# Kernel optimization log

Measured on AMD Instinct MI355X. Metric: run time of the kernel, lower is better.

The kernel has to match this reference:

```python
import jax, jax.numpy as jnp
import numpy as np

N, E = 20000, 160000
D_IN, HID, HEADS = 256, 64, 10
NEG_SLOPE = 0.2


def setup_inputs() -> dict:
    key = jax.random.key(0)
    ks = jax.random.split(key, 12)
    s = 0.05
    f = jnp.float32
    return {
        "x": jax.random.normal(ks[0], (N, D_IN), f),
        "edge_index": jax.random.randint(ks[1], (2, E), 0, N, jnp.int32),
        # GATConv 1: in=D_IN, out=HID, heads=10, concat=True
        "W1": (jax.random.normal(ks[2], (D_IN, HEADS * HID), f) * s),
        "a_src1": (jax.random.normal(ks[3], (HEADS, HID), f) * s),
        "a_dst1": (jax.random.normal(ks[4], (HEADS, HID), f) * s),
        "b1": jnp.zeros((HEADS * HID,), f),
        # GATConv 2: in=HEADS*HID, out=HID, heads=1
        "W2": (jax.random.normal(ks[5], (HEADS * HID, HID), f) * s),
        "a_src2": (jax.random.normal(ks[6], (1, HID), f) * s),
        "a_dst2": (jax.random.normal(ks[7], (1, HID), f) * s),
        "b2": jnp.zeros((HID,), f),
        # final Linear(hidden_dim, hidden_dim)
        "Wfc": (jax.random.normal(ks[8], (HID, HID), f) * s),
        "bfc": jnp.zeros((HID,), f),
    }


def gat_conv(x, src, dst, n, W, a_src, a_dst, b, heads, concat):
    """PyG GATConv (eval mode): gather, leaky-relu scores, segment softmax, scatter."""
    c = W.shape[1] // heads
    h = (x @ W).reshape(n, heads, c)                      # [N, H, C]
    score_src = jnp.sum(h * a_src, axis=-1)               # [N, H]
    score_dst = jnp.sum(h * a_dst, axis=-1)               # [N, H]
    e = jax.nn.leaky_relu(score_src[src] + score_dst[dst], NEG_SLOPE)  # [E, H]
    # segment softmax over incoming edges of each dst node
    m = jax.ops.segment_max(e, dst, num_segments=n)
    e = jnp.exp(e - m[dst])
    denom = jax.ops.segment_sum(e, dst, num_segments=n)
    alpha = e / (denom[dst] + 1e-16)                      # [E, H]
    msg = alpha[:, :, None] * h[src]                      # [E, H, C]
    out = jax.ops.segment_sum(msg, dst, num_segments=n)   # [N, H, C]
    out = out.reshape(n, heads * c) if concat else out.mean(axis=1)
    return out + b


def reference(x, edge_index, W1, a_src1, a_dst1, b1, W2, a_src2, a_dst2, b2, Wfc, bfc):
    n = x.shape[0]
    # add self loops (PyG default)
    loops = jnp.arange(n, dtype=edge_index.dtype)
    src = jnp.concatenate([edge_index[0], loops])
    dst = jnp.concatenate([edge_index[1], loops])
    h = jax.nn.relu(gat_conv(x, src, dst, n, W1, a_src1, a_dst1, b1, HEADS, True))
    h = jax.nn.relu(gat_conv(h, src, dst, n, W2, a_src2, a_dst2, b2, 1, True))
    return jax.nn.relu(h @ Wfc + bfc)
```

## Files before the change

kernel.cpp:

```cpp
#include <hip/hip_runtime.h>
#include <cstdint>
#include <cstddef>

constexpr int N_NODES = 20000;
constexpr int E_EDGES = 160000;
constexpr int D_INC   = 256;
constexpr int HEADSC  = 10;
constexpr int EN      = E_EDGES + N_NODES;
constexpr int ELLW    = 96;
constexpr float NEG_SLOPE = 0.2f;

typedef _Float16 half8 __attribute__((ext_vector_type(8)));
typedef _Float16 half4v __attribute__((ext_vector_type(4)));
typedef float f32x4 __attribute__((ext_vector_type(4)));

typedef const __attribute__((address_space(1))) void* gas_ptr;
typedef __attribute__((address_space(3))) void* las_ptr;

__global__ __launch_bounds__(256) void gemm1_k(
    const _Float16* __restrict__ A,
    const _Float16* __restrict__ BT,
    _Float16* __restrict__ C,
    const float* __restrict__ asv, const float* __restrict__ adv,
    float* __restrict__ s_s, float* __restrict__ s_d, int M)
{
    __shared__ alignas(16) _Float16 Ah[128][64];
    __shared__ alignas(16) _Float16 Bh[128][64];
    const int tid = threadIdx.x;
    const int wv  = tid >> 6;
    const int ln  = tid & 63;
    const int wr  = wv >> 1;
    const int wc  = wv & 1;
    const int row0 = blockIdx.y * 128;
    const int col0 = blockIdx.x * 128;
    const int m = ln & 15;
    const int q = ln >> 4;
    const int srow = tid >> 3;
    const int sk   = (tid & 7) * 8;

    f32x4 acc[4][4] = {};

    for (int k0 = 0; k0 < 256; k0 += 64) {
#pragma unroll
        for (int u = 0; u < 4; ++u) {
            const int ar = min(row0 + u * 32 + srow, M - 1);
            __builtin_amdgcn_global_load_lds(
                (gas_ptr)(A + (size_t)ar * 256 + k0 + sk),
                (las_ptr)(&Ah[u * 32 + srow][sk]), 16, 0, 0);
        }
#pragma unroll
        for (int u = 0; u < 4; ++u) {
            __builtin_amdgcn_global_load_lds(
                (gas_ptr)(BT + (size_t)(col0 + u * 32 + srow) * 256 + k0 + sk),
                (las_ptr)(&Bh[u * 32 + srow][sk]), 16, 0, 0);
        }
        __syncthreads();

#pragma unroll
        for (int ks = 0; ks < 2; ++ks) {
            half8 af[4], bf[4];
#pragma unroll
            for (int i = 0; i < 4; ++i)
                af[i] = *reinterpret_cast<const half8*>(
                    &Ah[wr * 64 + i * 16 + m][ks * 32 + q * 8]);
#pragma unroll
            for (int j = 0; j < 4; ++j)
                bf[j] = *reinterpret_cast<const half8*>(
                    &Bh[wc * 64 + j * 16 + m][ks * 32 + q * 8]);
#pragma unroll
            for (int i = 0; i < 4; ++i)
#pragma unroll
                for (int j = 0; j < 4; ++j)
                    acc[i][j] = __builtin_amdgcn_mfma_f32_16x16x32_f16(
                        af[i], bf[j], acc[i][j], 0, 0, 0);
        }
        __syncthreads();
    }

#pragma unroll
    for (int i = 0; i < 4; ++i) {
#pragma unroll
        for (int j = 0; j < 4; ++j) {
            const int col = col0 + wc * 64 + j * 16 + m;
#pragma unroll
            for (int r = 0; r < 4; ++r) {
                const int row = row0 + wr * 64 + i * 16 + q * 4 + r;
                if (row < M)
                    C[(size_t)row * 640 + col] = (_Float16)acc[i][j][r];
            }
        }
    }

    const int hh = blockIdx.x * 2 + wc;
    float pa[4][4] = {}, pd[4][4] = {};
#pragma unroll
    for (int j = 0; j < 4; ++j) {
        const float a_ = asv[hh * 64 + j * 16 + m];
        const float d_ = adv[hh * 64 + j * 16 + m];
#pragma unroll
        for (int i = 0; i < 4; ++i)
#pragma unroll
            for (int r = 0; r < 4; ++r) {
                pa[i][r] += acc[i][j][r] * a_;
                pd[i][r] += acc[i][j][r] * d_;
            }
    }
#pragma unroll
    for (int o = 1; o < 16; o <<= 1) {
#pragma unroll
        for (int i = 0; i < 4; ++i)
#pragma unroll
            for (int r = 0; r < 4; ++r) {
                pa[i][r] += __shfl_xor(pa[i][r], o, 64);
                pd[i][r] += __shfl_xor(pd[i][r], o, 64);
            }
    }
    if (m == 0) {
#pragma unroll
        for (int i = 0; i < 4; ++i)
#pragma unroll
            for (int r = 0; r < 4; ++r) {
                const int row = row0 + wr * 64 + i * 16 + q * 4 + r;
                if (row < M) {
                    s_s[row * HEADSC + hh] = pa[i][r];
                    s_d[row * HEADSC + hh] = pd[i][r];
                }
            }
    }
}

__global__ __launch_bounds__(128) void gemm2_k(
    const _Float16* __restrict__ A,
    const _Float16* __restrict__ BT,
    _Float16* __restrict__ C,
    const float* __restrict__ asv, const float* __restrict__ adv,
    float* __restrict__ s_s, float* __restrict__ s_d)
{
    __shared__ alignas(16) _Float16 Ah[32][72];
    __shared__ alignas(16) _Float16 Bh[64][72];
    const int tid = threadIdx.x;
    const int wv  = tid >> 6;
    const int ln  = tid & 63;
    const int row0 = blockIdx.x * 32;
    const int m = ln & 15;
    const int q = ln >> 4;
    const int arow = tid >> 2;
    const int acg  = (tid & 3) * 16;
    const int brow = tid >> 1;
    const int bcg  = (tid & 1) * 32;

    const _Float16* aptr = A  + (size_t)(row0 + arow) * 640 + acg;
    const _Float16* bptr = BT + (size_t)brow * 640 + bcg;

    int4 a0, a1, b0, b1, b2, b3;
    a0 = *reinterpret_cast<const int4*>(aptr);
    a1 = *reinterpret_cast<const int4*>(aptr + 8);
    b0 = *reinterpret_cast<const int4*>(bptr);
    b1 = *reinterpret_cast<const int4*>(bptr + 8);
    b2 = *reinterpret_cast<const int4*>(bptr + 16);
    b3 = *reinterpret_cast<const int4*>(bptr + 24);

    f32x4 acc[4] = {};

    for (int k0 = 0; k0 < 640; k0 += 64) {
        *reinterpret_cast<int4*>(&Ah[arow][acg])      = a0;
        *reinterpret_cast<int4*>(&Ah[arow][acg + 8])  = a1;
        *reinterpret_cast<int4*>(&Bh[brow][bcg])      = b0;
        *reinterpret_cast<int4*>(&Bh[brow][bcg + 8])  = b1;
        *reinterpret_cast<int4*>(&Bh[brow][bcg + 16]) = b2;
        *reinterpret_cast<int4*>(&Bh[brow][bcg + 24]) = b3;
        __syncthreads();

        if (k0 + 64 < 640) {
            const _Float16* ap = aptr + k0 + 64;
            a0 = *reinterpret_cast<const int4*>(ap);
            a1 = *reinterpret_cast<const int4*>(ap + 8);
            const _Float16* bp = bptr + k0 + 64;
            b0 = *reinterpret_cast<const int4*>(bp);
            b1 = *reinterpret_cast<const int4*>(bp + 8);
            b2 = *reinterpret_cast<const int4*>(bp + 16);
            b3 = *reinterpret_cast<const int4*>(bp + 24);
        }

#pragma unroll
        for (int ks = 0; ks < 2; ++ks) {
            const half8 af = *reinterpret_cast<const half8*>(
                &Ah[wv * 16 + m][ks * 32 + q * 8]);
#pragma unroll
            for (int ct = 0; ct < 4; ++ct) {
                const half8 bf = *reinterpret_cast<const half8*>(
                    &Bh[ct * 16 + m][ks * 32 + q * 8]);
                acc[ct] = __builtin_amdgcn_mfma_f32_16x16x32_f16(af, bf, acc[ct],
                                                                 0, 0, 0);
            }
        }
        __syncthreads();
    }

#pragma unroll
    for (int ct = 0; ct < 4; ++ct) {
#pragma unroll
        for (int r = 0; r < 4; ++r) {
            const int row = row0 + wv * 16 + q * 4 + r;
            C[(size_t)row * 64 + ct * 16 + m] = (_Float16)acc[ct][r];
        }
    }

    float pa[4] = {}, pd[4] = {};
#pragma unroll
    for (int ct = 0; ct < 4; ++ct) {
        const float a_ = asv[ct * 16 + m];
        const float d_ = adv[ct * 16 + m];
#pragma unroll
        for (int r = 0; r < 4; ++r) {
            pa[r] += acc[ct][r] * a_;
            pd[r] += acc[ct][r] * d_;
        }
    }
#pragma unroll
    for (int o = 1; o < 16; o <<= 1) {
#pragma unroll
        for (int r = 0; r < 4; ++r) {
            pa[r] += __shfl_xor(pa[r], o, 64);
            pd[r] += __shfl_xor(pd[r], o, 64);
        }
    }
    if (m == 0) {
#pragma unroll
        for (int r = 0; r < 4; ++r) {
            const int row = row0 + wv * 16 + q * 4 + r;
            s_s[row] = pa[r];
            s_d[row] = pd[r];
        }
    }
}

constexpr int XQ   = N_NODES * D_INC / 4;
constexpr int W1E  = D_INC * 640;
constexpr int W2E  = 640 * 64;
constexpr int WFCE = 64 * 64;
constexpr int SETUP_TOT = EN + XQ + W1E + W2E + WFCE;

__global__ void setup_k(const int* __restrict__ src, const int* __restrict__ dst,
                        int* __restrict__ deg, int* __restrict__ ell,
                        const float* __restrict__ x, const float* __restrict__ W1,
                        const float* __restrict__ W2, const float* __restrict__ Wfc,
                        _Float16* __restrict__ x16, _Float16* __restrict__ W1T,
                        _Float16* __restrict__ W2T, _Float16* __restrict__ WfcT)
{
    const int i = blockIdx.x * 256 + threadIdx.x;
    if (i < EN) {
        const int base = deg[N_NODES];
        int d, s;
        if (i < E_EDGES) { d = dst[i]; s = src[i]; }
        else             { d = i - E_EDGES; s = d; }
        const int r = atomicAdd(&deg[d], 1) - base;
        if ((unsigned)r < (unsigned)ELLW) ell[(size_t)d * ELLW + r] = s;
    } else if (i < EN + XQ) {
        const int j = i - EN;
        const float4 v = reinterpret_cast<const float4*>(x)[j];
        half4v o = {(_Float16)v.x, (_Float16)v.y, (_Float16)v.z, (_Float16)v.w};
        reinterpret_cast<half4v*>(x16)[j] = o;
    } else if (i < EN + XQ + W1E) {
        const int j = i - EN - XQ;
        const int k = j / 640, n = j - k * 640;
        W1T[(size_t)n * D_INC + k] = (_Float16)W1[j];
    } else if (i < EN + XQ + W1E + W2E) {
        const int j = i - EN - XQ - W1E;
        const int k = j / 64, n = j - k * 64;
        W2T[(size_t)n * 640 + k] = (_Float16)W2[j];
    } else if (i < SETUP_TOT) {
        const int j = i - EN - XQ - W1E - W2E;
        const int k = j >> 6, n = j & 63;
        WfcT[(size_t)n * 64 + k] = (_Float16)Wfc[j];
    }
}

__global__ __launch_bounds__(320) void agg_f16_oct(
    const _Float16* __restrict__ h, const float* __restrict__ s_s,
    const float* __restrict__ s_d, const int* __restrict__ deg,
    const int* __restrict__ ell, const float* __restrict__ bias,
    _Float16* __restrict__ outp)
{
    const int t   = blockIdx.x * 320 + threadIdx.x;
    const int n   = t / 80;
    const int oct = t - n * 80;
    if (n >= N_NODES) return;
    const int hh  = oct >> 3;
    const _Float16* __restrict__ hb = h + oct * 8;
    const int* __restrict__ row = ell + (size_t)n * ELLW;
    const float sd = s_d[n * HEADSC + hh];
    const int dbase = deg[N_NODES];
    const int dc = min(deg[n] - dbase, ELLW);

    float acc[8] = {};
    float den = 0.f;
    int i = 0;
    for (; i + 3 < dc; i += 4) {
        const int s0 = row[i], s1 = row[i + 1], s2 = row[i + 2], s3 = row[i + 3];
        const float g0 = s_s[s0 * HEADSC + hh], g1 = s_s[s1 * HEADSC + hh];
        const float g2 = s_s[s2 * HEADSC + hh], g3 = s_s[s3 * HEADSC + hh];
        const half8 v0 = *reinterpret_cast<const half8*>(hb + (size_t)s0 * 640);
        const half8 v1 = *reinterpret_cast<const half8*>(hb + (size_t)s1 * 640);
        const half8 v2 = *reinterpret_cast<const half8*>(hb + (size_t)s2 * 640);
        const half8 v3 = *reinterpret_cast<const half8*>(hb + (size_t)s3 * 640);
        float e0 = g0 + sd, e1 = g1 + sd, e2 = g2 + sd, e3 = g3 + sd;
        e0 = (e0 > 0.f) ? e0 : NEG_SLOPE * e0;
        e1 = (e1 > 0.f) ? e1 : NEG_SLOPE * e1;
        e2 = (e2 > 0.f) ? e2 : NEG_SLOPE * e2;
        e3 = (e3 > 0.f) ? e3 : NEG_SLOPE * e3;
        const float w0 = __expf(e0), w1 = __expf(e1);
        const float w2 = __expf(e2), w3 = __expf(e3);
        den += (w0 + w1) + (w2 + w3);
#pragma unroll
        for (int j = 0; j < 8; ++j)
            acc[j] += (w0 * (float)v0[j] + w1 * (float)v1[j])
                    + (w2 * (float)v2[j] + w3 * (float)v3[j]);
    }
    for (; i < dc; ++i) {
        const int s0 = row[i];
        const float g0 = s_s[s0 * HEADSC + hh];
        const half8 v0 = *reinterpret_cast<const half8*>(hb + (size_t)s0 * 640);
        float e0 = g0 + sd;
        e0 = (e0 > 0.f) ? e0 : NEG_SLOPE * e0;
        const float w0 = __expf(e0);
        den += w0;
#pragma unroll
        for (int j = 0; j < 8; ++j) acc[j] += w0 * (float)v0[j];
    }
    const float inv = 1.f / (den + 1e-16f);
    const float* bb = bias + oct * 8;
    half8 o;
#pragma unroll
    for (int j = 0; j < 8; ++j)
        o[j] = (_Float16)fmaxf(acc[j] * inv + bb[j], 0.f);
    *reinterpret_cast<half8*>(outp + (size_t)n * 640 + oct * 8) = o;
}

__global__ __launch_bounds__(256) void agg2fc_k(
    const _Float16* __restrict__ h,
    const float* __restrict__ s_s, const float* __restrict__ s_d,
    const int* __restrict__ deg, const int* __restrict__ ell,
    const float* __restrict__ b2,
    const _Float16* __restrict__ WfcT,
    const float* __restrict__ bfc,
    float* __restrict__ out)
{
    __shared__ alignas(16) _Float16 Os[32][72];
    const int tid = threadIdx.x;
    const int n0  = blockIdx.x * 32;
    const int nl  = tid >> 3;
    const int oct = tid & 7;
    const int n   = n0 + nl;

    {
        const _Float16* __restrict__ hb = h + oct * 8;
        const int* __restrict__ row = ell + (size_t)n * ELLW;
        const float sd = s_d[n];
        const int dbase = deg[N_NODES];
        const int dc = min(deg[n] - dbase, ELLW);

        float acc[8] = {};
        float den = 0.f;
        int i = 0;
        for (; i + 3 < dc; i += 4) {
            int   sv[4];
            float gv[4];
            half8 hv[4];
#pragma unroll
            for (int u = 0; u < 4; ++u) sv[u] = row[i + u];
#pragma unroll
            for (int u = 0; u < 4; ++u) gv[u] = s_s[sv[u]];
#pragma unroll
            for (int u = 0; u < 4; ++u)
                hv[u] = *reinterpret_cast<const half8*>(hb + (size_t)sv[u] * 64);
#pragma unroll
            for (int u = 0; u < 4; ++u) {
                float e = gv[u] + sd;
                e = (e > 0.f) ? e : NEG_SLOPE * e;
                const float w = __expf(e);
                den += w;
#pragma unroll
                for (int j = 0; j < 8; ++j) acc[j] += w * (float)hv[u][j];
            }
        }
        for (; i < dc; ++i) {
            const int s0 = row[i];
            const float g0 = s_s[s0];
            const half8 v0 = *reinterpret_cast<const half8*>(hb + (size_t)s0 * 64);
            float e0 = g0 + sd;
            e0 = (e0 > 0.f) ? e0 : NEG_SLOPE * e0;
            const float w0 = __expf(e0);
            den += w0;
#pragma unroll
            for (int j = 0; j < 8; ++j) acc[j] += w0 * (float)v0[j];
        }
        const float inv = 1.f / (den + 1e-16f);
        const float* bb = b2 + oct * 8;
        half8 o;
#pragma unroll
        for (int j = 0; j < 8; ++j)
            o[j] = (_Float16)fmaxf(acc[j] * inv + bb[j], 0.f);
        *reinterpret_cast<half8*>(&Os[nl][oct * 8]) = o;
    }
    __syncthreads();

    const int wv = tid >> 6;
    const int ln = tid & 63;
    if (wv < 2) {
        const int m = ln & 15;
        const int q = ln >> 4;
        f32x4 acc[4] = {};
#pragma unroll
        for (int ks = 0; ks < 2; ++ks) {
            const half8 af = *reinterpret_cast<const half8*>(
                &Os[wv * 16 + m][ks * 32 + q * 8]);
#pragma unroll
            for (int ct = 0; ct < 4; ++ct) {
                const half8 bf = *reinterpret_cast<const half8*>(
                    WfcT + (size_t)(ct * 16 + m) * 64 + ks * 32 + q * 8);
                acc[ct] = __builtin_amdgcn_mfma_f32_16x16x32_f16(af, bf, acc[ct],
                                                                 0, 0, 0);
            }
        }
#pragma unroll
        for (int ct = 0; ct < 4; ++ct) {
#pragma unroll
            for (int r = 0; r < 4; ++r) {
                const int row = n0 + wv * 16 + q * 4 + r;
                const int col = ct * 16 + m;
                out[(size_t)row * 64 + col] = fmaxf(acc[ct][r] + bfc[col], 0.f);
            }
        }
    }
}

extern "C" void kernel_launch(void* const* d_in, const int* in_sizes, int n_in,
                              void* d_out, int out_size, void* d_ws, size_t ws_size,
                              hipStream_t stream)
{
    const float* x      = (const float*)d_in[0];
    const int*   edges  = (const int*)d_in[1];
    const float* W1     = (const float*)d_in[2];
    const float* a_src1 = (const float*)d_in[3];
    const float* a_dst1 = (const float*)d_in[4];
    const float* b1     = (const float*)d_in[5];
    const float* W2     = (const float*)d_in[6];
    const float* a_src2 = (const float*)d_in[7];
    const float* a_dst2 = (const float*)d_in[8];
    const float* b2     = (const float*)d_in[9];
    const float* Wfc    = (const float*)d_in[10];
    const float* bfc    = (const float*)d_in[11];
    float* out = (float*)d_out;

    const int* src = edges;
    const int* dst = edges + E_EDGES;

    char* ws = (char*)d_ws;
    size_t off = 0;
    auto alloc = [&](size_t bytes) -> void* {
        void* p = ws + off;
        off += (bytes + 255) & ~(size_t)255;
        return p;
    };
    _Float16*  h1   = (_Float16*)alloc((size_t)N_NODES * 640 * sizeof(_Float16));
    _Float16*  out1 = (_Float16*)alloc((size_t)N_NODES * 640 * sizeof(_Float16));
    _Float16*  h2   = (_Float16*)alloc((size_t)N_NODES * 64 * sizeof(_Float16));
    _Float16*  x16  = (_Float16*)alloc((size_t)N_NODES * D_INC * sizeof(_Float16));
    _Float16*  W1T  = (_Float16*)alloc((size_t)640 * D_INC * sizeof(_Float16));
    _Float16*  W2T  = (_Float16*)alloc((size_t)64 * 640 * sizeof(_Float16));
    _Float16*  WfcT = (_Float16*)alloc((size_t)64 * 64 * sizeof(_Float16));
    float*     ss1  = (float*)alloc((size_t)N_NODES * HEADSC * sizeof(float));
    float*     sd1  = (float*)alloc((size_t)N_NODES * HEADSC * sizeof(float));
    float*     ss2  = (float*)alloc((size_t)N_NODES * sizeof(float));
    float*     sd2  = (float*)alloc((size_t)N_NODES * sizeof(float));
    int*       deg  = (int*)alloc((size_t)(N_NODES + 1) * sizeof(int));
    int*       ell  = (int*)alloc((size_t)N_NODES * ELLW * sizeof(int));

    setup_k<<<(SETUP_TOT + 255) / 256, 256, 0, stream>>>(
        src, dst, deg, ell, x, W1, W2, Wfc, x16, W1T, W2T, WfcT);

    dim3 g1(5, (N_NODES + 127) / 128);
    gemm1_k<<<g1, 256, 0, stream>>>(x16, W1T, h1, a_src1, a_dst1,
                                    ss1, sd1, N_NODES);

    agg_f16_oct<<<(N_NODES * 80) / 320, 320, 0, stream>>>(h1, ss1, sd1, deg, ell,
                                                          b1, out1);

    gemm2_k<<<N_NODES / 32, 128, 0, stream>>>(out1, W2T, h2, a_src2, a_dst2,
                                              ss2, sd2);

    agg2fc_k<<<N_NODES / 32, 256, 0, stream>>>(h2, ss2, sd2, deg, ell,
                                               b2, WfcT, bfc, out);
}
```

Measured before the change: 179.0 us.

## Fuse layer-1 aggregation with layer-2 GEMM and attention scores

Merges the layer-1 neighbor aggregation kernel with the layer-2 projection GEMM. Each 320-thread block aggregates 4 nodes into shared memory. One wave then runs MFMAs against W2T read directly from global memory and writes h2 plus the layer-2 source and destination scores. This removes the full out1 intermediate write and read and one kernel launch. In exchange, 12 of the 16 MFMA rows are wasted on uninitialised shared rows, the whole W2T is re-read from cache by every block, and four of the five waves sit idle during the GEMM phase.

```diff
diff --git a/kernel.cpp b/kernel.cpp
--- a/kernel.cpp
+++ b/kernel.cpp
@@ -126,112 +126,6 @@
                     s_d[row * HEADSC + hh] = pd[i][r];
                 }
             }
-    }
-}
-
-__global__ __launch_bounds__(128) void gemm2_k(
-    const _Float16* __restrict__ A,
-    const _Float16* __restrict__ BT,
-    _Float16* __restrict__ C,
-    const float* __restrict__ asv, const float* __restrict__ adv,
-    float* __restrict__ s_s, float* __restrict__ s_d)
-{
-    __shared__ alignas(16) _Float16 Ah[32][72];
-    __shared__ alignas(16) _Float16 Bh[64][72];
-    const int tid = threadIdx.x;
-    const int wv  = tid >> 6;
-    const int ln  = tid & 63;
-    const int row0 = blockIdx.x * 32;
-    const int m = ln & 15;
-    const int q = ln >> 4;
-    const int arow = tid >> 2;
-    const int acg  = (tid & 3) * 16;
-    const int brow = tid >> 1;
-    const int bcg  = (tid & 1) * 32;
-
-    const _Float16* aptr = A  + (size_t)(row0 + arow) * 640 + acg;
-    const _Float16* bptr = BT + (size_t)brow * 640 + bcg;
-
-    int4 a0, a1, b0, b1, b2, b3;
-    a0 = *reinterpret_cast<const int4*>(aptr);
-    a1 = *reinterpret_cast<const int4*>(aptr + 8);
-    b0 = *reinterpret_cast<const int4*>(bptr);
-    b1 = *reinterpret_cast<const int4*>(bptr + 8);
-    b2 = *reinterpret_cast<const int4*>(bptr + 16);
-    b3 = *reinterpret_cast<const int4*>(bptr + 24);
-
-    f32x4 acc[4] = {};
-
-    for (int k0 = 0; k0 < 640; k0 += 64) {
-        *reinterpret_cast<int4*>(&Ah[arow][acg])      = a0;
-        *reinterpret_cast<int4*>(&Ah[arow][acg + 8])  = a1;
-        *reinterpret_cast<int4*>(&Bh[brow][bcg])      = b0;
-        *reinterpret_cast<int4*>(&Bh[brow][bcg + 8])  = b1;
-        *reinterpret_cast<int4*>(&Bh[brow][bcg + 16]) = b2;
-        *reinterpret_cast<int4*>(&Bh[brow][bcg + 24]) = b3;
-        __syncthreads();
-
-        if (k0 + 64 < 640) {
-            const _Float16* ap = aptr + k0 + 64;
-            a0 = *reinterpret_cast<const int4*>(ap);
-            a1 = *reinterpret_cast<const int4*>(ap + 8);
-            const _Float16* bp = bptr + k0 + 64;
-            b0 = *reinterpret_cast<const int4*>(bp);
-            b1 = *reinterpret_cast<const int4*>(bp + 8);
-            b2 = *reinterpret_cast<const int4*>(bp + 16);
-            b3 = *reinterpret_cast<const int4*>(bp + 24);
-        }
-
-#pragma unroll
-        for (int ks = 0; ks < 2; ++ks) {
-            const half8 af = *reinterpret_cast<const half8*>(
-                &Ah[wv * 16 + m][ks * 32 + q * 8]);
-#pragma unroll
-            for (int ct = 0; ct < 4; ++ct) {
-                const half8 bf = *reinterpret_cast<const half8*>(
-                    &Bh[ct * 16 + m][ks * 32 + q * 8]);
-                acc[ct] = __builtin_amdgcn_mfma_f32_16x16x32_f16(af, bf, acc[ct],
-                                                                 0, 0, 0);
-            }
-        }
-        __syncthreads();
-    }
-
-#pragma unroll
-    for (int ct = 0; ct < 4; ++ct) {
-#pragma unroll
-        for (int r = 0; r < 4; ++r) {
-            const int row = row0 + wv * 16 + q * 4 + r;
-            C[(size_t)row * 64 + ct * 16 + m] = (_Float16)acc[ct][r];
-        }
-    }
-
-    float pa[4] = {}, pd[4] = {};
-#pragma unroll
-    for (int ct = 0; ct < 4; ++ct) {
-        const float a_ = asv[ct * 16 + m];
-        const float d_ = adv[ct * 16 + m];
-#pragma unroll
-        for (int r = 0; r < 4; ++r) {
-            pa[r] += acc[ct][r] * a_;
-            pd[r] += acc[ct][r] * d_;
-        }
-    }
-#pragma unroll
-    for (int o = 1; o < 16; o <<= 1) {
-#pragma unroll
-        for (int r = 0; r < 4; ++r) {
-            pa[r] += __shfl_xor(pa[r], o, 64);
-            pd[r] += __shfl_xor(pd[r], o, 64);
-        }
-    }
-    if (m == 0) {
-#pragma unroll
-        for (int r = 0; r < 4; ++r) {
-            const int row = row0 + wv * 16 + q * 4 + r;
-            s_s[row] = pa[r];
-            s_d[row] = pd[r];
-        }
     }
 }
 
@@ -276,65 +170,126 @@
     }
 }
 
-__global__ __launch_bounds__(320) void agg_f16_oct(
-    const _Float16* __restrict__ h, const float* __restrict__ s_s,
-    const float* __restrict__ s_d, const int* __restrict__ deg,
-    const int* __restrict__ ell, const float* __restrict__ bias,
-    _Float16* __restrict__ outp)
+__global__ __launch_bounds__(320) void agg1g2_k(
+    const _Float16* __restrict__ h,
+    const float* __restrict__ s_s, const float* __restrict__ s_d,
+    const int* __restrict__ deg, const int* __restrict__ ell,
+    const float* __restrict__ bias,
+    const _Float16* __restrict__ W2T,
+    const float* __restrict__ asv2, const float* __restrict__ adv2,
+    _Float16* __restrict__ h2,
+    float* __restrict__ ss2, float* __restrict__ sd2)
 {
-    const int t   = blockIdx.x * 320 + threadIdx.x;
-    const int n   = t / 80;
-    const int oct = t - n * 80;
-    if (n >= N_NODES) return;
-    const int hh  = oct >> 3;
-    const _Float16* __restrict__ hb = h + oct * 8;
-    const int* __restrict__ row = ell + (size_t)n * ELLW;
-    const float sd = s_d[n * HEADSC + hh];
-    const int dbase = deg[N_NODES];
-    const int dc = min(deg[n] - dbase, ELLW);
-
-    float acc[8] = {};
-    float den = 0.f;
-    int i = 0;
-    for (; i + 3 < dc; i += 4) {
-        const int s0 = row[i], s1 = row[i + 1], s2 = row[i + 2], s3 = row[i + 3];
-        const float g0 = s_s[s0 * HEADSC + hh], g1 = s_s[s1 * HEADSC + hh];
-        const float g2 = s_s[s2 * HEADSC + hh], g3 = s_s[s3 * HEADSC + hh];
-        const half8 v0 = *reinterpret_cast<const half8*>(hb + (size_t)s0 * 640);
-        const half8 v1 = *reinterpret_cast<const half8*>(hb + (size_t)s1 * 640);
-        const half8 v2 = *reinterpret_cast<const half8*>(hb + (size_t)s2 * 640);
-        const half8 v3 = *reinterpret_cast<const half8*>(hb + (size_t)s3 * 640);
-        float e0 = g0 + sd, e1 = g1 + sd, e2 = g2 + sd, e3 = g3 + sd;
-        e0 = (e0 > 0.f) ? e0 : NEG_SLOPE * e0;
-        e1 = (e1 > 0.f) ? e1 : NEG_SLOPE * e1;
-        e2 = (e2 > 0.f) ? e2 : NEG_SLOPE * e2;
-        e3 = (e3 > 0.f) ? e3 : NEG_SLOPE * e3;
-        const float w0 = __expf(e0), w1 = __expf(e1);
-        const float w2 = __expf(e2), w3 = __expf(e3);
-        den += (w0 + w1) + (w2 + w3);
+    __shared__ alignas(16) _Float16 Os[16][648];
+    const int tid = threadIdx.x;
+    const int nl  = tid / 80;
+    const int oct = tid - nl * 80;
+    const int n0  = blockIdx.x * 4;
+    const int n   = n0 + nl;
+
+    {
+        const int hh  = oct >> 3;
+        const _Float16* __restrict__ hb = h + oct * 8;
+        const int* __restrict__ row = ell + (size_t)n * ELLW;
+        const float sd = s_d[n * HEADSC + hh];
+        const int dbase = deg[N_NODES];
+        const int dc = min(deg[n] - dbase, ELLW);
+
+        float acc[8] = {};
+        float den = 0.f;
+        int i = 0;
+        for (; i + 3 < dc; i += 4) {
+            const int s0 = row[i], s1 = row[i + 1], s2 = row[i + 2], s3 = row[i + 3];
+            const float g0 = s_s[s0 * HEADSC + hh], g1 = s_s[s1 * HEADSC + hh];
+            const float g2 = s_s[s2 * HEADSC + hh], g3 = s_s[s3 * HEADSC + hh];
+            const half8 v0 = *reinterpret_cast<const half8*>(hb + (size_t)s0 * 640);
+            const half8 v1 = *reinterpret_cast<const half8*>(hb + (size_t)s1 * 640);
+            const half8 v2 = *reinterpret_cast<const half8*>(hb + (size_t)s2 * 640);
+            const half8 v3 = *reinterpret_cast<const half8*>(hb + (size_t)s3 * 640);
+            float e0 = g0 + sd, e1 = g1 + sd, e2 = g2 + sd, e3 = g3 + sd;
+            e0 = (e0 > 0.f) ? e0 : NEG_SLOPE * e0;
+            e1 = (e1 > 0.f) ? e1 : NEG_SLOPE * e1;
+            e2 = (e2 > 0.f) ? e2 : NEG_SLOPE * e2;
+            e3 = (e3 > 0.f) ? e3 : NEG_SLOPE * e3;
+            const float w0 = __expf(e0), w1 = __expf(e1);
+            const float w2 = __expf(e2), w3 = __expf(e3);
+            den += (w0 + w1) + (w2 + w3);
+#pragma unroll
+            for (int j = 0; j < 8; ++j)
+                acc[j] += (w0 * (float)v0[j] + w1 * (float)v1[j])
+                        + (w2 * (float)v2[j] + w3 * (float)v3[j]);
+        }
+        for (; i < dc; ++i) {
+            const int s0 = row[i];
+            const float g0 = s_s[s0 * HEADSC + hh];
+            const half8 v0 = *reinterpret_cast<const half8*>(hb + (size_t)s0 * 640);
+            float e0 = g0 + sd;
+            e0 = (e0 > 0.f) ? e0 : NEG_SLOPE * e0;
+            const float w0 = __expf(e0);
+            den += w0;
+#pragma unroll
+            for (int j = 0; j < 8; ++j) acc[j] += w0 * (float)v0[j];
+        }
+        const float inv = 1.f / (den + 1e-16f);
+        const float* bb = bias + oct * 8;
+        half8 o;
 #pragma unroll
         for (int j = 0; j < 8; ++j)
-            acc[j] += (w0 * (float)v0[j] + w1 * (float)v1[j])
-                    + (w2 * (float)v2[j] + w3 * (float)v3[j]);
-    }
-    for (; i < dc; ++i) {
-        const int s0 = row[i];
-        const float g0 = s_s[s0 * HEADSC + hh];
-        const half8 v0 = *reinterpret_cast<const half8*>(hb + (size_t)s0 * 640);
-        float e0 = g0 + sd;
-        e0 = (e0 > 0.f) ? e0 : NEG_SLOPE * e0;
-        const float w0 = __expf(e0);
-        den += w0;
-#pragma unroll
-        for (int j = 0; j < 8; ++j) acc[j] += w0 * (float)v0[j];
-    }
-    const float inv = 1.f / (den + 1e-16f);
-    const float* bb = bias + oct * 8;
-    half8 o;
-#pragma unroll
-    for (int j = 0; j < 8; ++j)
-        o[j] = (_Float16)fmaxf(acc[j] * inv + bb[j], 0.f);
-    *reinterpret_cast<half8*>(outp + (size_t)n * 640 + oct * 8) = o;
+            o[j] = (_Float16)fmaxf(acc[j] * inv + bb[j], 0.f);
+        *reinterpret_cast<half8*>(&Os[nl][oct * 8]) = o;
+    }
+    __syncthreads();
+
+    if (tid < 64) {
+        const int m = tid & 15;
+        const int q = tid >> 4;
+        f32x4 a2[4] = {};
+#pragma unroll 4
+        for (int ks = 0; ks < 20; ++ks) {
+            const half8 af = *reinterpret_cast<const half8*>(
+                &Os[m][ks * 32 + q * 8]);
+#pragma unroll
+            for (int ct = 0; ct < 4; ++ct) {
+                const half8 bf = *reinterpret_cast<const half8*>(
+                    W2T + (size_t)(ct * 16 + m) * 640 + ks * 32 + q * 8);
+                a2[ct] = __builtin_amdgcn_mfma_f32_16x16x32_f16(af, bf, a2[ct],
+                                                                0, 0, 0);
+            }
+        }
+        if (q == 0) {
+#pragma unroll
+            for (int ct = 0; ct < 4; ++ct)
+#pragma unroll
+                for (int r = 0; r < 4; ++r)
+                    h2[(size_t)(n0 + r) * 64 + ct * 16 + m] = (_Float16)a2[ct][r];
+        }
+        float pa[4] = {}, pd[4] = {};
+#pragma unroll
+        for (int ct = 0; ct < 4; ++ct) {
+            const float a_ = asv2[ct * 16 + m];
+            const float d_ = adv2[ct * 16 + m];
+#pragma unroll
+            for (int r = 0; r < 4; ++r) {
+                pa[r] += a2[ct][r] * a_;
+                pd[r] += a2[ct][r] * d_;
+            }
+        }
+#pragma unroll
+        for (int o = 1; o < 16; o <<= 1) {
+#pragma unroll
+            for (int r = 0; r < 4; ++r) {
+                pa[r] += __shfl_xor(pa[r], o, 64);
+                pd[r] += __shfl_xor(pd[r], o, 64);
+            }
+        }
+        if (tid == 0) {
+#pragma unroll
+            for (int r = 0; r < 4; ++r) {
+                ss2[n0 + r] = pa[r];
+                sd2[n0 + r] = pd[r];
+            }
+        }
+    }
 }
 
 __global__ __launch_bounds__(256) void agg2fc_k(
@@ -464,7 +419,6 @@
         return p;
     };
     _Float16*  h1   = (_Float16*)alloc((size_t)N_NODES * 640 * sizeof(_Float16));
-    _Float16*  out1 = (_Float16*)alloc((size_t)N_NODES * 640 * sizeof(_Float16));
     _Float16*  h2   = (_Float16*)alloc((size_t)N_NODES * 64 * sizeof(_Float16));
     _Float16*  x16  = (_Float16*)alloc((size_t)N_NODES * D_INC * sizeof(_Float16));
     _Float16*  W1T  = (_Float16*)alloc((size_t)640 * D_INC * sizeof(_Float16));
@@ -484,11 +438,9 @@
     gemm1_k<<<g1, 256, 0, stream>>>(x16, W1T, h1, a_src1, a_dst1,
                                     ss1, sd1, N_NODES);
 
-    agg_f16_oct<<<(N_NODES * 80) / 320, 320, 0, stream>>>(h1, ss1, sd1, deg, ell,
-                                                          b1, out1);
-
-    gemm2_k<<<N_NODES / 32, 128, 0, stream>>>(out1, W2T, h2, a_src2, a_dst2,
-                                              ss2, sd2);
+    agg1g2_k<<<N_NODES / 4, 320, 0, stream>>>(h1, ss1, sd1, deg, ell, b1,
+                                              W2T, a_src2, a_dst2,
+                                              h2, ss2, sd2);
 
     agg2fc_k<<<N_NODES / 32, 256, 0, stream>>>(h2, ss2, sd2, deg, ell,
                                                b2, WfcT, bfc, out);
```

After: 202.7 us. +13.2%, slower.
